# Kernel optimization log

Measured on AMD Instinct MI355X. Metric: run time of the kernel, lower is better.

The kernel has to match this reference:

```python
import jax, jax.numpy as jnp
import numpy as np

B = 2048   # batch
C = 64     # EEG channels (num_eegch)
T = 125    # time samples -> pool5 -> 25 -> (p=5, 5)
H = 8      # num_heads
L = 6      # num_layers
D = 16     # num_projected_features
QK = 8     # qkv_len
P = 5      # tokens before cls
EPS = 1e-5


def setup_inputs() -> dict:
    key = jax.random.key(0)
    ks = iter(jax.random.split(key, 64))

    def nrm(shape, s=0.05):
        return jax.random.normal(next(ks), shape, jnp.float32) * s

    return {
        "x": jax.random.normal(next(ks), (B, 1, C, T), jnp.float32),
        "conv_t_w": nrm((8, 1, 1, 63)),
        "conv_t_b": nrm((8,)),
        "bn1_g": 1.0 + nrm((8,)),
        "bn1_b": nrm((8,)),
        "bn1_m": nrm((8,)),
        "bn1_v": 1.0 + 0.1 * jax.random.uniform(next(ks), (8,), jnp.float32),
        "conv_s_w": nrm((16, 1, C, 1)),
        "conv_s_b": nrm((16,)),
        "bn2_g": 1.0 + nrm((16,)),
        "bn2_b": nrm((16,)),
        "bn2_m": nrm((16,)),
        "bn2_v": 1.0 + 0.1 * jax.random.uniform(next(ks), (16,), jnp.float32),
        "proj_w": nrm((D, 16 * 5)),
        "proj_b": nrm((D,)),
        "cls_token": nrm((1, 1, D), 1.0),
        "pe": nrm((1, P + 1, D), 1.0),
        "qkv_w": nrm((L, 3 * H * QK, D)),
        "qkv_b": nrm((L, 3 * H * QK)),
        "out_w": nrm((L, D, H * QK)),
        "out_b": nrm((L, D)),
        "ln1_g": jnp.ones((L, D), jnp.float32),
        "ln1_b": jnp.zeros((L, D), jnp.float32),
        "ln2_g": jnp.ones((L, D), jnp.float32),
        "ln2_b": jnp.zeros((L, D), jnp.float32),
        "mlp_w1": nrm((L, 2 * D, D)),
        "mlp_b1": nrm((L, 2 * D)),
        "mlp_w2": nrm((L, D, 2 * D)),
        "mlp_b2": nrm((L, D)),
        "head_ln_g": jnp.ones((D,), jnp.float32),
        "head_ln_b": jnp.zeros((D,), jnp.float32),
        "head_w": nrm((2, D)),
        "head_b": nrm((2,)),
    }


def _bn(z, g, b, m, v):
    s = (g * jax.lax.rsqrt(v + EPS))[None, :, None, None]
    return (z - m[None, :, None, None]) * s + b[None, :, None, None]


def _ln(z, g, b):
    m = z.mean(-1, keepdims=True)
    var = jnp.mean((z - m) ** 2, -1, keepdims=True)
    return (z - m) * jax.lax.rsqrt(var + EPS) * g + b


def _forward(x, conv_t_w, conv_t_b, bn1_g, bn1_b, bn1_m, bn1_v,
             conv_s_w, conv_s_b, bn2_g, bn2_b, bn2_m, bn2_v,
             proj_w, proj_b, cls_token, pe,
             qkv_w, qkv_b, out_w, out_b, ln1_g, ln1_b, ln2_g, ln2_b,
             mlp_w1, mlp_b1, mlp_w2, mlp_b2,
             head_ln_g, head_ln_b, head_w, head_b):
    b = x.shape[0]
    dn = ('NCHW', 'OIHW', 'NCHW')
    # temporal conv, 'same' padding on width (kernel 63 -> pad 31/31)
    y = jax.lax.conv_general_dilated(x, conv_t_w, (1, 1), [(0, 0), (31, 31)], dimension_numbers=dn)
    y = _bn(y + conv_t_b[None, :, None, None], bn1_g, bn1_b, bn1_m, bn1_v)
    # grouped spatial conv collapses the EEG-channel axis
    y = jax.lax.conv_general_dilated(y, conv_s_w, (1, 1), 'VALID', dimension_numbers=dn, feature_group_count=8)
    y = _bn(y + conv_s_b[None, :, None, None], bn2_g, bn2_b, bn2_m, bn2_v)
    y = jax.nn.elu(y)                              # (b,16,1,125)
    y = y.reshape(b, 16, 1, T // 5, 5).mean(-1)    # avg_pool2d (1,5) -> (b,16,1,25)
    # dropout: identity at inference
    y = y.reshape(b, 16, 1, P, 5)
    y = jnp.swapaxes(y, 3, 4)
    tok = jnp.swapaxes(y.reshape(b, 16 * 5, P), 1, 2)   # (b,5,80)
    tok = tok @ proj_w.T + proj_b                       # (b,5,16)
    z = jnp.concatenate([jnp.broadcast_to(cls_token, (b, 1, D)), tok], axis=1) + pe  # (b,6,16)
    scale = QK ** -0.5
    for i in range(L):
        h1 = _ln(z, ln1_g[i], ln1_b[i])
        qkv = h1 @ qkv_w[i].T + qkv_b[i]                # (b,6,3*H*QK)
        q, k, v = jnp.split(qkv, 3, axis=-1)
        q = q.reshape(b, P + 1, H, QK).transpose(0, 2, 1, 3)
        k = k.reshape(b, P + 1, H, QK).transpose(0, 2, 1, 3)
        v = v.reshape(b, P + 1, H, QK).transpose(0, 2, 1, 3)
        att = jax.nn.softmax(jnp.einsum('bhsd,bhtd->bhst', q, k) * scale, axis=-1)
        o = jnp.einsum('bhst,bhtd->bhsd', att, v).transpose(0, 2, 1, 3).reshape(b, P + 1, H * QK)
        z = o @ out_w[i].T + out_b[i] + z
        h2 = _ln(z, ln2_g[i], ln2_b[i])
        m = jax.nn.gelu(h2 @ mlp_w1[i].T + mlp_b1[i], approximate=False) @ mlp_w2[i].T + mlp_b2[i]
        z = m + z
    cls = _ln(z[:, 0, :], head_ln_g, head_ln_b)
    return jax.nn.softmax(cls @ head_w.T + head_b, axis=-1)


def reference(x, conv_t_w, conv_t_b, bn1_g, bn1_b, bn1_m, bn1_v,
              conv_s_w, conv_s_b, bn2_g, bn2_b, bn2_m, bn2_v,
              proj_w, proj_b, cls_token, pe,
              qkv_w, qkv_b, out_w, out_b, ln1_g, ln1_b, ln2_g, ln2_b,
              mlp_w1, mlp_b1, mlp_w2, mlp_b2,
              head_ln_g, head_ln_b, head_w, head_b):
    return _forward(x, conv_t_w, conv_t_b, bn1_g, bn1_b, bn1_m, bn1_v,
                    conv_s_w, conv_s_b, bn2_g, bn2_b, bn2_m, bn2_v,
                    proj_w, proj_b, cls_token, pe,
                    qkv_w, qkv_b, out_w, out_b, ln1_g, ln1_b, ln2_g, ln2_b,
                    mlp_w1, mlp_b1, mlp_w2, mlp_b2,
                    head_ln_g, head_ln_b, head_w, head_b)
```

## Files before the change

### kernel.cpp

```cpp
#include <hip/hip_runtime.h>

#define WAVE_SYNC() do { asm volatile("" ::: "memory"); \
                         __builtin_amdgcn_wave_barrier(); \
                         asm volatile("" ::: "memory"); } while (0)

typedef _Float16 h2 __attribute__((ext_vector_type(2)));
typedef _Float16 h4 __attribute__((ext_vector_type(4)));
typedef _Float16 h8 __attribute__((ext_vector_type(8)));

__device__ __forceinline__ float fdot2(h2 a, h2 b, float c) {
#if defined(__has_builtin)
#if __has_builtin(__builtin_amdgcn_fdot2)
    return __builtin_amdgcn_fdot2(a, b, c, false);
#else
    return (float)a[0]*(float)b[0] + (float)a[1]*(float)b[1] + c;
#endif
#else
    return (float)a[0]*(float)b[0] + (float)a[1]*(float)b[1] + c;
#endif
}

__device__ __forceinline__ float dot8h(h8 a, h8 b, float c) {
    float s = c;
    #pragma unroll
    for (int i = 0; i < 4; ++i) {
        h2 x = {a[2*i], a[2*i+1]};
        h2 y = {b[2*i], b[2*i+1]};
        s = fdot2(x, y, s);
    }
    return s;
}

__device__ __forceinline__ float dot16h(h8 a0, h8 a1, h8 b0, h8 b1, float c) {
    return dot8h(a1, b1, dot8h(a0, b0, c));
}

__device__ __forceinline__ float ln_norm16(float z, float g, float bb) {
    float s = z, q = z * z;
    #pragma unroll
    for (int off = 8; off >= 1; off >>= 1) {
        s += __shfl_xor(s, off, 16);
        q += __shfl_xor(q, off, 16);
    }
    float mean = s * 0.0625f;
    float var  = q * 0.0625f - mean * mean;
    return (z - mean) * rsqrtf(var + 1e-5f) * g + bb;
}

__device__ __forceinline__ float gelu_exact(float a) {
    float xa = fabsf(a) * 0.70710678118654752f;
    float tt = 1.f / (1.f + 0.3275911f * xa);
    float poly = tt * (0.254829592f + tt * (-0.284496736f + tt * (1.421413741f
               + tt * (-1.453152027f + tt * 1.061405429f))));
    float erfv = 1.f - poly * __expf(-xa * xa);
    erfv = a >= 0.f ? erfv : -erfv;
    return 0.5f * a * (1.f + erfv);
}

#define FS_XSTR 210
#define FS_PF   1680
#define FS_TOTF 2128

extern "C" __global__ __launch_bounds__(128, 2)
void eegnet_frontend(
    const float* __restrict__ x,
    const float* __restrict__ conv_t_w, const float* __restrict__ conv_t_b,
    const float* __restrict__ bn1_g, const float* __restrict__ bn1_b,
    const float* __restrict__ bn1_m, const float* __restrict__ bn1_v,
    const float* __restrict__ conv_s_w, const float* __restrict__ conv_s_b,
    const float* __restrict__ bn2_g, const float* __restrict__ bn2_b,
    const float* __restrict__ bn2_m, const float* __restrict__ bn2_v,
    const float* __restrict__ proj_w, const float* __restrict__ proj_b,
    float* __restrict__ tokws)
{
    __shared__ __align__(16) float sm[FS_TOTF];
    _Float16* smh = reinterpret_cast<_Float16*>(sm);
    const int b   = blockIdx.x;
    const int tid = threadIdx.x;

    for (int i = tid; i < 16 * 85; i += 128) {
        int row = i / 85, k = i - row * 85;
        int off = (k < 32) ? k : (k + 125);
        smh[row * FS_XSTR + off] = (_Float16)0.f;
    }

    if (tid < 125) {
        const float* xb = x + (size_t)b * 8000 + tid;
        float acc[16];
        #pragma unroll
        for (int o = 0; o < 16; ++o) acc[o] = 0.f;
        #pragma unroll 8
        for (int c = 0; c < 64; ++c) {
            float xv = xb[c * 125];
            #pragma unroll
            for (int o = 0; o < 16; ++o)
                acc[o] += conv_s_w[o * 64 + c] * xv;
        }
        #pragma unroll
        for (int o = 0; o < 16; ++o)
            smh[o * FS_XSTR + 32 + tid] = (_Float16)acc[o];
    }

    __syncthreads();

    const int oo = tid & 15, qg = tid >> 4, gg = oo >> 1;
    float sa, cc;
    {
        float s1 = bn1_g[gg] * rsqrtf(bn1_v[gg] + 1e-5f);
        float b1 = (conv_t_b[gg] - bn1_m[gg]) * s1 + bn1_b[gg];
        float s2 = bn2_g[oo] * rsqrtf(bn2_v[oo] + 1e-5f);
        float ssum = 0.f;
        const float4* csw = reinterpret_cast<const float4*>(conv_s_w + oo * 64);
        #pragma unroll
        for (int i = 0; i < 16; ++i) {
            float4 v = csw[i];
            ssum += v.x + v.y + v.z + v.w;
        }
        sa = s1 * s2;
        cc = (b1 * ssum + conv_s_b[oo] - bn2_m[oo]) * s2 + bn2_b[oo];
    }
    float wt[63];
    #pragma unroll
    for (int k = 0; k < 63; ++k) wt[k] = conv_t_w[gg * 63 + k];

    #pragma unroll 2
    for (int jj = 0; jj < 4; ++jj) {
        int j  = qg * 4 + jj;
        int jc = min(j, 24);
        int base = oo * FS_XSTR + 5 * jc + 1;
        float acc5[5] = {0.f, 0.f, 0.f, 0.f, 0.f};
        #pragma unroll
        for (int m = 0; m < 67; ++m) {
            float xv = (float)smh[base + m];
            #pragma unroll
            for (int u = 0; u < 5; ++u)
                if (u <= m && m - u <= 62) acc5[u] += wt[m - u] * xv;
        }
        float psum = 0.f;
        #pragma unroll
        for (int u = 0; u < 5; ++u) {
            float v = acc5[u] * sa + cc;
            psum += (v > 0.f) ? v : (__expf(v) - 1.f);
        }
        if (j == jc) sm[FS_PF + oo * 28 + j] = psum * 0.2f;
    }

    __syncthreads();

    if (tid < 80) {
        int p = tid >> 4, dd = tid & 15;
        float acc = proj_b[dd];
        const float4* wp = reinterpret_cast<const float4*>(proj_w + dd * 80);
        #pragma unroll
        for (int i = 0; i < 20; ++i) {
            float4 w4 = wp[i];
            acc += w4.x * sm[FS_PF + ((4*i+0)/5) * 28 + p * 5 + ((4*i+0)%5)];
            acc += w4.y * sm[FS_PF + ((4*i+1)/5) * 28 + p * 5 + ((4*i+1)%5)];
            acc += w4.z * sm[FS_PF + ((4*i+2)/5) * 28 + p * 5 + ((4*i+2)%5)];
            acc += w4.w * sm[FS_PF + ((4*i+3)/5) * 28 + p * 5 + ((4*i+3)%5)];
        }
        tokws[b * 80 + p * 16 + dd] = acc;
    }
}

#define WQKVH 0
#define WOUTH 4608
#define WM1H  5760
#define WM2H  6528
#define BQKVF 3584
#define BOUTF 3776
#define BM1F  3792
#define BM2F  3824
#define LN1GF 3840
#define LN1BF 3856
#define LN2GF 3872
#define LN2BF 3888
#define SCR0  7808
#define SSTRH 1584
#define SH1H  0
#define SQKVH 144
#define SMHSH 1344
#define T_BYTES 28288

extern "C" __global__ __launch_bounds__(256, 2)
void eegnet_transformer(
    const float* __restrict__ cls_token, const float* __restrict__ pe,
    const float* __restrict__ qkv_w, const float* __restrict__ qkv_b,
    const float* __restrict__ out_w, const float* __restrict__ out_b,
    const float* __restrict__ ln1_g, const float* __restrict__ ln1_b,
    const float* __restrict__ ln2_g, const float* __restrict__ ln2_b,
    const float* __restrict__ mlp_w1, const float* __restrict__ mlp_b1,
    const float* __restrict__ mlp_w2, const float* __restrict__ mlp_b2,
    const float* __restrict__ head_ln_g, const float* __restrict__ head_ln_b,
    const float* __restrict__ head_w, const float* __restrict__ head_b,
    const float* __restrict__ tokws, float* __restrict__ out)
{
    __shared__ __align__(16) unsigned char smb[T_BYTES];
    float*    smf = reinterpret_cast<float*>(smb);
    _Float16* smh = reinterpret_cast<_Float16*>(smb);

    const int tid = threadIdx.x;
    const int ss  = tid >> 7;
    const int u   = tid & 127;
    const int sA  = blockIdx.x * 4 + ss * 2;
    const int d16 = u & 15, qg = u >> 4;
    const int t6c = min(qg, 5);
    const int wav = u >> 6, al = u & 63;
    const int sbA = SCR0 + (ss * 2    ) * SSTRH;
    const int sbB = SCR0 + (ss * 2 + 1) * SSTRH;

    float zA, zB;
    {
        float peV = pe[t6c * 16 + d16];
        if (t6c == 0) {
            float cv = cls_token[d16];
            zA = cv + peV; zB = cv + peV;
        } else {
            zA = tokws[(sA    ) * 80 + (t6c - 1) * 16 + d16] + peV;
            zB = tokws[(sA + 1) * 80 + (t6c - 1) * 16 + d16] + peV;
        }
    }

    #pragma unroll 1
    for (int li = 0; li < 6; ++li) {
        __syncthreads();

        {
            const float4* s1 = reinterpret_cast<const float4*>(qkv_w + li * 3072);
            #pragma unroll
            for (int it = 0; it < 3; ++it) {
                int i = tid + it * 256;
                float4 v = s1[i];
                int j = i >> 2, k = (i & 3) << 2;
                h4 hv = {(_Float16)v.x, (_Float16)v.y, (_Float16)v.z, (_Float16)v.w};
                *reinterpret_cast<h4*>(&smh[WQKVH + j * 24 + k]) = hv;
            }
            {
                float4 v = reinterpret_cast<const float4*>(out_w + li * 1024)[tid];
                int j = tid >> 4, k = (tid & 15) << 2;
                h4 hv = {(_Float16)v.x, (_Float16)v.y, (_Float16)v.z, (_Float16)v.w};
                *reinterpret_cast<h4*>(&smh[WOUTH + j * 72 + k]) = hv;
            }
            if (tid < 128) {
                float4 v = reinterpret_cast<const float4*>(mlp_w1 + li * 512)[tid];
                int j = tid >> 2, k = (tid & 3) << 2;
                h4 hv = {(_Float16)v.x, (_Float16)v.y, (_Float16)v.z, (_Float16)v.w};
                *reinterpret_cast<h4*>(&smh[WM1H + j * 24 + k]) = hv;
            } else {
                int i = tid - 128;
                float4 v = reinterpret_cast<const float4*>(mlp_w2 + li * 512)[i];
                int j = i >> 3, k = (i & 7) << 2;
                h4 hv = {(_Float16)v.x, (_Float16)v.y, (_Float16)v.z, (_Float16)v.w};
                *reinterpret_cast<h4*>(&smh[WM2H + j * 40 + k]) = hv;
            }
            if (tid < 192) smf[BQKVF + tid] = qkv_b[li * 192 + tid];
            else if (tid < 208) smf[BOUTF + tid - 192] = out_b[li * 16 + tid - 192];
            else if (tid < 240) smf[BM1F + tid - 208]  = mlp_b1[li * 32 + tid - 208];
            else               smf[BM2F + tid - 240]  = mlp_b2[li * 16 + tid - 240];
            if (tid >= 64 && tid < 80)        smf[LN1GF + tid - 64]  = ln1_g[li * 16 + tid - 64];
            else if (tid >= 80 && tid < 96)   smf[LN1BF + tid - 80]  = ln1_b[li * 16 + tid - 80];
            else if (tid >= 96 && tid < 112)  smf[LN2GF + tid - 96]  = ln2_g[li * 16 + tid - 96];
            else if (tid >= 112 && tid < 128) smf[LN2BF + tid - 112] = ln2_b[li * 16 + tid - 112];
        }
        __syncthreads();

        {
            float g = smf[LN1GF + d16], bb = smf[LN1BF + d16];
            smh[sbA + SH1H + t6c * 24 + d16] = (_Float16)ln_norm16(zA, g, bb);
            smh[sbB + SH1H + t6c * 24 + d16] = (_Float16)ln_norm16(zB, g, bb);
        }
        WAVE_SYNC();

        h8 hA0 = *reinterpret_cast<const h8*>(&smh[sbA + SH1H + t6c * 24]);
        h8 hA1 = *reinterpret_cast<const h8*>(&smh[sbA + SH1H + t6c * 24 + 8]);
        h8 hB0 = *reinterpret_cast<const h8*>(&smh[sbB + SH1H + t6c * 24]);
        h8 hB1 = *reinterpret_cast<const h8*>(&smh[sbB + SH1H + t6c * 24 + 8]);

        #pragma unroll 2
        for (int r = 0; r < 12; ++r) {
            int j = d16 + 16 * r;
            h8 w0 = *reinterpret_cast<const h8*>(&smh[WQKVH + j * 24]);
            h8 w1 = *reinterpret_cast<const h8*>(&smh[WQKVH + j * 24 + 8]);
            float bb = smf[BQKVF + j];
            smh[sbA + SQKVH + t6c * 200 + j] = (_Float16)dot16h(hA0, hA1, w0, w1, bb);
            smh[sbB + SQKVH + t6c * 200 + j] = (_Float16)dot16h(hB0, hB1, w0, w1, bb);
        }
        __syncthreads();

        {
            bool act = (wav == 0) ? (al < 32) : (al < 16);
            if (act) {
                int h  = al & 7;
                int qs = (wav == 0) ? (al >> 3) : 4 + (al >> 3);
                const int qoffA = sbA + SQKVH + qs * 200 + h * 8;
                const int qoffB = sbB + SQKVH + qs * 200 + h * 8;
                h8 qA = *reinterpret_cast<const h8*>(&smh[qoffA]);
                h8 qB = *reinterpret_cast<const h8*>(&smh[qoffB]);
                float scA[6], scB[6];
                #pragma unroll
                for (int t = 0; t < 6; ++t) {
                    h8 kA = *reinterpret_cast<const h8*>(&smh[sbA + SQKVH + t * 200 + 64 + h * 8]);
                    h8 kB = *reinterpret_cast<const h8*>(&smh[sbB + SQKVH + t * 200 + 64 + h * 8]);
                    scA[t] = dot8h(qA, kA, 0.f) * 0.35355339059327373f;
                    scB[t] = dot8h(qB, kB, 0.f) * 0.35355339059327373f;
                }
                float mxA = scA[0], mxB = scB[0];
                #pragma unroll
                for (int t = 1; t < 6; ++t) { mxA = fmaxf(mxA, scA[t]); mxB = fmaxf(mxB, scB[t]); }
                float suA = 0.f, suB = 0.f;
                #pragma unroll
                for (int t = 0; t < 6; ++t) {
                    scA[t] = __expf(scA[t] - mxA); suA += scA[t];
                    scB[t] = __expf(scB[t] - mxB); suB += scB[t];
                }
                float ivA = 1.f / suA, ivB = 1.f / suB;
                h2 oA[4], oB[4];
                #pragma unroll
                for (int k2 = 0; k2 < 4; ++k2) { oA[k2] = h2{0, 0}; oB[k2] = h2{0, 0}; }
                #pragma unroll
                for (int t = 0; t < 6; ++t) {
                    h8 vA = *reinterpret_cast<const h8*>(&smh[sbA + SQKVH + t * 200 + 128 + h * 8]);
                    h8 vB = *reinterpret_cast<const h8*>(&smh[sbB + SQKVH + t * 200 + 128 + h * 8]);
                    _Float16 aa = (_Float16)(scA[t] * ivA);
                    _Float16 ab = (_Float16)(scB[t] * ivB);
                    h2 av = {aa, aa}, bv = {ab, ab};
                    #pragma unroll
                    for (int k2 = 0; k2 < 4; ++k2) {
                        h2 va = {vA[2*k2], vA[2*k2+1]};
                        h2 vb = {vB[2*k2], vB[2*k2+1]};
                        oA[k2] += av * va;
                        oB[k2] += bv * vb;
                    }
                }
                h8 stA, stB;
                #pragma unroll
                for (int k2 = 0; k2 < 4; ++k2) {
                    stA[2*k2] = oA[k2][0]; stA[2*k2+1] = oA[k2][1];
                    stB[2*k2] = oB[k2][0]; stB[2*k2+1] = oB[k2][1];
                }
                *reinterpret_cast<h8*>(&smh[qoffA]) = stA;
                *reinterpret_cast<h8*>(&smh[qoffB]) = stB;
            }
        }
        WAVE_SYNC();

        {
            float aA = smf[BOUTF + d16], aB = aA;
            #pragma unroll
            for (int i = 0; i < 8; ++i) {
                h8 w  = *reinterpret_cast<const h8*>(&smh[WOUTH + d16 * 72 + 8 * i]);
                h8 va = *reinterpret_cast<const h8*>(&smh[sbA + SQKVH + t6c * 200 + 8 * i]);
                h8 vb = *reinterpret_cast<const h8*>(&smh[sbB + SQKVH + t6c * 200 + 8 * i]);
                aA = dot8h(va, w, aA);
                aB = dot8h(vb, w, aB);
            }
            zA += aA; zB += aB;
        }

        {
            float g = smf[LN2GF + d16], bb = smf[LN2BF + d16];
            smh[sbA + SH1H + t6c * 24 + d16] = (_Float16)ln_norm16(zA, g, bb);
            smh[sbB + SH1H + t6c * 24 + d16] = (_Float16)ln_norm16(zB, g, bb);
        }
        WAVE_SYNC();
        hA0 = *reinterpret_cast<const h8*>(&smh[sbA + SH1H + t6c * 24]);
        hA1 = *reinterpret_cast<const h8*>(&smh[sbA + SH1H + t6c * 24 + 8]);
        hB0 = *reinterpret_cast<const h8*>(&smh[sbB + SH1H + t6c * 24]);
        hB1 = *reinterpret_cast<const h8*>(&smh[sbB + SH1H + t6c * 24 + 8]);

        #pragma unroll
        for (int r = 0; r < 2; ++r) {
            int uu = d16 + 16 * r;
            h8 w0 = *reinterpret_cast<const h8*>(&smh[WM1H + uu * 24]);
            h8 w1 = *reinterpret_cast<const h8*>(&smh[WM1H + uu * 24 + 8]);
            float bb = smf[BM1F + uu];
            float aA = dot16h(hA0, hA1, w0, w1, bb);
            float aB = dot16h(hB0, hB1, w0, w1, bb);
            smh[sbA + SMHSH + t6c * 40 + uu] = (_Float16)gelu_exact(aA);
            smh[sbB + SMHSH + t6c * 40 + uu] = (_Float16)gelu_exact(aB);
        }
        WAVE_SYNC();

        {
            float aA = smf[BM2F + d16], aB = aA;
            #pragma unroll
            for (int i = 0; i < 4; ++i) {
                h8 w  = *reinterpret_cast<const h8*>(&smh[WM2H + d16 * 40 + 8 * i]);
                h8 va = *reinterpret_cast<const h8*>(&smh[sbA + SMHSH + t6c * 40 + 8 * i]);
                h8 vb = *reinterpret_cast<const h8*>(&smh[sbB + SMHSH + t6c * 40 + 8 * i]);
                aA = dot8h(va, w, aA);
                aB = dot8h(vb, w, aB);
            }
            zA += aA; zB += aB;
        }
    }

    if (u < 16) {
        float g = head_ln_g[d16], bb = head_ln_b[d16];
        float w0 = head_w[d16], w1 = head_w[16 + d16];
        float cvA = ln_norm16(zA, g, bb);
        float cvB = ln_norm16(zB, g, bb);
        float pA0 = cvA * w0, pA1 = cvA * w1;
        float pB0 = cvB * w0, pB1 = cvB * w1;
        #pragma unroll
        for (int off = 8; off >= 1; off >>= 1) {
            pA0 += __shfl_xor(pA0, off, 16);
            pA1 += __shfl_xor(pA1, off, 16);
            pB0 += __shfl_xor(pB0, off, 16);
            pB1 += __shfl_xor(pB1, off, 16);
        }
        if (u == 0) {
            float hb0 = head_b[0], hb1 = head_b[1];
            {
                float l0 = pA0 + hb0, l1 = pA1 + hb1;
                float mx = fmaxf(l0, l1);
                float e0 = __expf(l0 - mx), e1 = __expf(l1 - mx);
                float inv = 1.f / (e0 + e1);
                out[sA * 2 + 0] = e0 * inv;
                out[sA * 2 + 1] = e1 * inv;
            }
            {
                float l0 = pB0 + hb0, l1 = pB1 + hb1;
                float mx = fmaxf(l0, l1);
                float e0 = __expf(l0 - mx), e1 = __expf(l1 - mx);
                float inv = 1.f / (e0 + e1);
                out[(sA + 1) * 2 + 0] = e0 * inv;
                out[(sA + 1) * 2 + 1] = e1 * inv;
            }
        }
    }
}

extern "C" void kernel_launch(void* const* d_in, const int* in_sizes, int n_in,
                              void* d_out, int out_size, void* d_ws, size_t ws_size,
                              hipStream_t stream) {
    (void)n_in; (void)ws_size; (void)out_size;
    const float* a0  = (const float*)d_in[0];
    const float* a1  = (const float*)d_in[1];
    const float* a2  = (const float*)d_in[2];
    const float* a3  = (const float*)d_in[3];
    const float* a4  = (const float*)d_in[4];
    const float* a5  = (const float*)d_in[5];
    const float* a6  = (const float*)d_in[6];
    const float* a7  = (const float*)d_in[7];
    const float* a8  = (const float*)d_in[8];
    const float* a9  = (const float*)d_in[9];
    const float* a10 = (const float*)d_in[10];
    const float* a11 = (const float*)d_in[11];
    const float* a12 = (const float*)d_in[12];
    const float* a13 = (const float*)d_in[13];
    const float* a14 = (const float*)d_in[14];
    const float* a15 = (const float*)d_in[15];
    const float* a16 = (const float*)d_in[16];
    const float* a17 = (const float*)d_in[17];
    const float* a18 = (const float*)d_in[18];
    const float* a19 = (const float*)d_in[19];
    const float* a20 = (const float*)d_in[20];
    const float* a21 = (const float*)d_in[21];
    const float* a22 = (const float*)d_in[22];
    const float* a23 = (const float*)d_in[23];
    const float* a24 = (const float*)d_in[24];
    const float* a25 = (const float*)d_in[25];
    const float* a26 = (const float*)d_in[26];
    const float* a27 = (const float*)d_in[27];
    const float* a28 = (const float*)d_in[28];
    const float* a29 = (const float*)d_in[29];
    const float* a30 = (const float*)d_in[30];
    const float* a31 = (const float*)d_in[31];
    const float* a32 = (const float*)d_in[32];

    int Bn = in_sizes[0] / (64 * 125);
    float* tokws = (float*)d_ws;

    eegnet_frontend<<<Bn, 128, 0, stream>>>(
        a0, a1, a2, a3, a4, a5, a6, a7, a8, a9, a10, a11, a12, a13, a14, tokws);

    eegnet_transformer<<<Bn / 4, 256, 0, stream>>>(
        a15, a16, a17, a18, a19, a20, a21, a22, a23, a24, a25, a26, a27, a28,
        a29, a30, a31, a32, tokws, (float*)d_out);
}
```

Before: 243.8 us.

## Stage input in LDS as fp16 for spatial conv; one sample per transformer block

The frontend now loads the whole per-sample input with vectorized float4 reads into shared memory as fp16. It also stages the spatial conv weights there and computes the channel conv with fdot2 instead of strided scalar global loads. The transformer kernel is restructured from 4 samples per 256-thread block (2 per thread) down to 1 sample per 128-thread block, with 4x more blocks. This trades weight-loading amortization across samples for more blocks and less LDS per block, and it lowers precision of the spatial conv inputs to fp16.

Result: no change. 240.0 us (-1.6%).

```diff
diff --git a/kernel.cpp b/kernel.cpp
--- a/kernel.cpp
+++ b/kernel.cpp
@@ -57,9 +57,10 @@
     return 0.5f * a * (1.f + erfv);
 }
 
-#define FS_XSTR 210
-#define FS_PF   1680
-#define FS_TOTF 2128
+#define F5_XSTR 210
+#define F5_PF   1680
+#define F5_WLH  8000
+#define F5_TOTF 4512
 
 extern "C" __global__ __launch_bounds__(128, 2)
 void eegnet_frontend(
@@ -73,34 +74,67 @@
     const float* __restrict__ proj_w, const float* __restrict__ proj_b,
     float* __restrict__ tokws)
 {
-    __shared__ __align__(16) float sm[FS_TOTF];
+    __shared__ __align__(16) float sm[F5_TOTF];
     _Float16* smh = reinterpret_cast<_Float16*>(sm);
     const int b   = blockIdx.x;
     const int tid = threadIdx.x;
 
+    {
+        const float4* xb4 = reinterpret_cast<const float4*>(x + (size_t)b * 8000);
+        #pragma unroll
+        for (int k = 0; k < 16; ++k) {
+            int g = min(tid + k * 128, 1999);
+            float4 v = xb4[g];
+            h4 hv = {(_Float16)v.x, (_Float16)v.y, (_Float16)v.z, (_Float16)v.w};
+            *reinterpret_cast<h4*>(&smh[4 * g]) = hv;
+        }
+    }
+    {
+        #pragma unroll
+        for (int k = 0; k < 4; ++k) {
+            int i  = tid + k * 128;
+            int c2 = i & 31, o = i >> 5;
+            float2 wv = *reinterpret_cast<const float2*>(conv_s_w + o * 64 + 2 * c2);
+            h2 hp = {(_Float16)wv.x, (_Float16)wv.y};
+            *reinterpret_cast<h2*>(&smh[F5_WLH + (c2 * 16 + o) * 2]) = hp;
+        }
+    }
+    __syncthreads();
+
+    float acc[16];
+    #pragma unroll
+    for (int o = 0; o < 16; ++o) acc[o] = 0.f;
+    if (tid < 125) {
+        #pragma unroll 4
+        for (int c2 = 0; c2 < 32; ++c2) {
+            h2 xp = { smh[(2 * c2) * 125 + tid], smh[(2 * c2 + 1) * 125 + tid] };
+            const h8* wrow = reinterpret_cast<const h8*>(&smh[F5_WLH + c2 * 32]);
+            h8 w0 = wrow[0], w1 = wrow[1], w2 = wrow[2], w3 = wrow[3];
+            #pragma unroll
+            for (int o = 0; o < 4; ++o) {
+                h2 p0 = {w0[2*o], w0[2*o+1]};
+                h2 p1 = {w1[2*o], w1[2*o+1]};
+                h2 p2 = {w2[2*o], w2[2*o+1]};
+                h2 p3 = {w3[2*o], w3[2*o+1]};
+                acc[o]      = fdot2(p0, xp, acc[o]);
+                acc[4 + o]  = fdot2(p1, xp, acc[4 + o]);
+                acc[8 + o]  = fdot2(p2, xp, acc[8 + o]);
+                acc[12 + o] = fdot2(p3, xp, acc[12 + o]);
+            }
+        }
+    }
+    __syncthreads();
+
     for (int i = tid; i < 16 * 85; i += 128) {
         int row = i / 85, k = i - row * 85;
         int off = (k < 32) ? k : (k + 125);
-        smh[row * FS_XSTR + off] = (_Float16)0.f;
-    }
-
+        smh[row * F5_XSTR + off] = (_Float16)0.f;
+    }
     if (tid < 125) {
-        const float* xb = x + (size_t)b * 8000 + tid;
-        float acc[16];
-        #pragma unroll
-        for (int o = 0; o < 16; ++o) acc[o] = 0.f;
-        #pragma unroll 8
-        for (int c = 0; c < 64; ++c) {
-            float xv = xb[c * 125];
-            #pragma unroll
-            for (int o = 0; o < 16; ++o)
-                acc[o] += conv_s_w[o * 64 + c] * xv;
-        }
         #pragma unroll
         for (int o = 0; o < 16; ++o)
-            smh[o * FS_XSTR + 32 + tid] = (_Float16)acc[o];
-    }
-
+            smh[o * F5_XSTR + 32 + tid] = (_Float16)acc[o];
+    }
     __syncthreads();
 
     const int oo = tid & 15, qg = tid >> 4, gg = oo >> 1;
@@ -127,7 +161,7 @@
     for (int jj = 0; jj < 4; ++jj) {
         int j  = qg * 4 + jj;
         int jc = min(j, 24);
-        int base = oo * FS_XSTR + 5 * jc + 1;
+        int base = oo * F5_XSTR + 5 * jc + 1;
         float acc5[5] = {0.f, 0.f, 0.f, 0.f, 0.f};
         #pragma unroll
         for (int m = 0; m < 67; ++m) {
@@ -142,24 +176,24 @@
             float v = acc5[u] * sa + cc;
             psum += (v > 0.f) ? v : (__expf(v) - 1.f);
         }
-        if (j == jc) sm[FS_PF + oo * 28 + j] = psum * 0.2f;
+        if (j == jc) sm[F5_PF + oo * 28 + j] = psum * 0.2f;
     }
 
     __syncthreads();
 
     if (tid < 80) {
         int p = tid >> 4, dd = tid & 15;
-        float acc = proj_b[dd];
+        float acc3 = proj_b[dd];
         const float4* wp = reinterpret_cast<const float4*>(proj_w + dd * 80);
         #pragma unroll
         for (int i = 0; i < 20; ++i) {
             float4 w4 = wp[i];
-            acc += w4.x * sm[FS_PF + ((4*i+0)/5) * 28 + p * 5 + ((4*i+0)%5)];
-            acc += w4.y * sm[FS_PF + ((4*i+1)/5) * 28 + p * 5 + ((4*i+1)%5)];
-            acc += w4.z * sm[FS_PF + ((4*i+2)/5) * 28 + p * 5 + ((4*i+2)%5)];
-            acc += w4.w * sm[FS_PF + ((4*i+3)/5) * 28 + p * 5 + ((4*i+3)%5)];
-        }
-        tokws[b * 80 + p * 16 + dd] = acc;
+            acc3 += w4.x * sm[F5_PF + ((4*i+0)/5) * 28 + p * 5 + ((4*i+0)%5)];
+            acc3 += w4.y * sm[F5_PF + ((4*i+1)/5) * 28 + p * 5 + ((4*i+1)%5)];
+            acc3 += w4.z * sm[F5_PF + ((4*i+2)/5) * 28 + p * 5 + ((4*i+2)%5)];
+            acc3 += w4.w * sm[F5_PF + ((4*i+3)/5) * 28 + p * 5 + ((4*i+3)%5)];
+        }
+        tokws[b * 80 + p * 16 + dd] = acc3;
     }
 }
 
@@ -180,9 +214,9 @@
 #define SH1H  0
 #define SQKVH 144
 #define SMHSH 1344
-#define T_BYTES 28288
-
-extern "C" __global__ __launch_bounds__(256, 2)
+#define T_BYTES 18784
+
+extern "C" __global__ __launch_bounds__(128, 2)
 void eegnet_transformer(
     const float* __restrict__ cls_token, const float* __restrict__ pe,
     const float* __restrict__ qkv_w, const float* __restrict__ qkv_b,
@@ -200,25 +234,17 @@
     _Float16* smh = reinterpret_cast<_Float16*>(smb);
 
     const int tid = threadIdx.x;
-    const int ss  = tid >> 7;
-    const int u   = tid & 127;
-    const int sA  = blockIdx.x * 4 + ss * 2;
-    const int d16 = u & 15, qg = u >> 4;
+    const int sA  = blockIdx.x;
+    const int d16 = tid & 15, qg = tid >> 4;
     const int t6c = min(qg, 5);
-    const int wav = u >> 6, al = u & 63;
-    const int sbA = SCR0 + (ss * 2    ) * SSTRH;
-    const int sbB = SCR0 + (ss * 2 + 1) * SSTRH;
-
-    float zA, zB;
+    const int wav = tid >> 6, al = tid & 63;
+    const int sb  = SCR0;
+
+    float zA;
     {
         float peV = pe[t6c * 16 + d16];
-        if (t6c == 0) {
-            float cv = cls_token[d16];
-            zA = cv + peV; zB = cv + peV;
-        } else {
-            zA = tokws[(sA    ) * 80 + (t6c - 1) * 16 + d16] + peV;
-            zB = tokws[(sA + 1) * 80 + (t6c - 1) * 16 + d16] + peV;
-        }
+        if (t6c == 0) zA = cls_token[d16] + peV;
+        else          zA = tokws[sA * 80 + (t6c - 1) * 16 + d16] + peV;
     }
 
     #pragma unroll 1
@@ -228,35 +254,42 @@
         {
             const float4* s1 = reinterpret_cast<const float4*>(qkv_w + li * 3072);
             #pragma unroll
-            for (int it = 0; it < 3; ++it) {
-                int i = tid + it * 256;
+            for (int it = 0; it < 6; ++it) {
+                int i = tid + it * 128;
                 float4 v = s1[i];
                 int j = i >> 2, k = (i & 3) << 2;
                 h4 hv = {(_Float16)v.x, (_Float16)v.y, (_Float16)v.z, (_Float16)v.w};
                 *reinterpret_cast<h4*>(&smh[WQKVH + j * 24 + k]) = hv;
             }
-            {
-                float4 v = reinterpret_cast<const float4*>(out_w + li * 1024)[tid];
-                int j = tid >> 4, k = (tid & 15) << 2;
+            const float4* s2 = reinterpret_cast<const float4*>(out_w + li * 1024);
+            #pragma unroll
+            for (int it = 0; it < 2; ++it) {
+                int i = tid + it * 128;
+                float4 v = s2[i];
+                int j = i >> 4, k = (i & 15) << 2;
                 h4 hv = {(_Float16)v.x, (_Float16)v.y, (_Float16)v.z, (_Float16)v.w};
                 *reinterpret_cast<h4*>(&smh[WOUTH + j * 72 + k]) = hv;
             }
-            if (tid < 128) {
+            {
                 float4 v = reinterpret_cast<const float4*>(mlp_w1 + li * 512)[tid];
                 int j = tid >> 2, k = (tid & 3) << 2;
                 h4 hv = {(_Float16)v.x, (_Float16)v.y, (_Float16)v.z, (_Float16)v.w};
                 *reinterpret_cast<h4*>(&smh[WM1H + j * 24 + k]) = hv;
-            } else {
-                int i = tid - 128;
-                float4 v = reinterpret_cast<const float4*>(mlp_w2 + li * 512)[i];
-                int j = i >> 3, k = (i & 7) << 2;
+            }
+            {
+                float4 v = reinterpret_cast<const float4*>(mlp_w2 + li * 512)[tid];
+                int j = tid >> 3, k = (tid & 7) << 2;
                 h4 hv = {(_Float16)v.x, (_Float16)v.y, (_Float16)v.z, (_Float16)v.w};
                 *reinterpret_cast<h4*>(&smh[WM2H + j * 40 + k]) = hv;
             }
-            if (tid < 192) smf[BQKVF + tid] = qkv_b[li * 192 + tid];
-            else if (tid < 208) smf[BOUTF + tid - 192] = out_b[li * 16 + tid - 192];
-            else if (tid < 240) smf[BM1F + tid - 208]  = mlp_b1[li * 32 + tid - 208];
-            else               smf[BM2F + tid - 240]  = mlp_b2[li * 16 + tid - 240];
+            #pragma unroll
+            for (int p = 0; p < 2; ++p) {
+                int i = tid + p * 128;
+                if (i < 192)       smf[BQKVF + i]       = qkv_b[li * 192 + i];
+                else if (i < 208)  smf[BOUTF + i - 192] = out_b[li * 16 + i - 192];
+                else if (i < 240)  smf[BM1F + i - 208]  = mlp_b1[li * 32 + i - 208];
+                else               smf[BM2F + i - 240]  = mlp_b2[li * 16 + i - 240];
+            }
             if (tid >= 64 && tid < 80)        smf[LN1GF + tid - 64]  = ln1_g[li * 16 + tid - 64];
             else if (tid >= 80 && tid < 96)   smf[LN1BF + tid - 80]  = ln1_b[li * 16 + tid - 80];
             else if (tid >= 96 && tid < 112)  smf[LN2GF + tid - 96]  = ln2_g[li * 16 + tid - 96];
@@ -266,15 +299,12 @@
 
         {
             float g = smf[LN1GF + d16], bb = smf[LN1BF + d16];
-            smh[sbA + SH1H + t6c * 24 + d16] = (_Float16)ln_norm16(zA, g, bb);
-            smh[sbB + SH1H + t6c * 24 + d16] = (_Float16)ln_norm16(zB, g, bb);
+            smh[sb + SH1H + t6c * 24 + d16] = (_Float16)ln_norm16(zA, g, bb);
         }
         WAVE_SYNC();
 
-        h8 hA0 = *reinterpret_cast<const h8*>(&smh[sbA + SH1H + t6c * 24]);
-        h8 hA1 = *reinterpret_cast<const h8*>(&smh[sbA + SH1H + t6c * 24 + 8]);
-        h8 hB0 = *reinterpret_cast<const h8*>(&smh[sbB + SH1H + t6c * 24]);
-        h8 hB1 = *reinterpret_cast<const h8*>(&smh[sbB + SH1H + t6c * 24 + 8]);
+        h8 hA0 = *reinterpret_cast<const h8*>(&smh[sb + SH1H + t6c * 24]);
+        h8 hA1 = *reinterpret_cast<const h8*>(&smh[sb + SH1H + t6c * 24 + 8]);
 
         #pragma unroll 2
         for (int r = 0; r < 12; ++r) {
@@ -282,8 +312,7 @@
             h8 w0 = *reinterpret_cast<const h8*>(&smh[WQKVH + j * 24]);
             h8 w1 = *reinterpret_cast<const h8*>(&smh[WQKVH + j * 24 + 8]);
             float bb = smf[BQKVF + j];
-            smh[sbA + SQKVH + t6c * 200 + j] = (_Float16)dot16h(hA0, hA1, w0, w1, bb);
-            smh[sbB + SQKVH + t6c * 200 + j] = (_Float16)dot16h(hB0, hB1, w0, w1, bb);
+            smh[sb + SQKVH + t6c * 200 + j] = (_Float16)dot16h(hA0, hA1, w0, w1, bb);
         }
         __syncthreads();
 
@@ -292,81 +321,63 @@
             if (act) {
                 int h  = al & 7;
                 int qs = (wav == 0) ? (al >> 3) : 4 + (al >> 3);
-                const int qoffA = sbA + SQKVH + qs * 200 + h * 8;
-                const int qoffB = sbB + SQKVH + qs * 200 + h * 8;
-                h8 qA = *reinterpret_cast<const h8*>(&smh[qoffA]);
-                h8 qB = *reinterpret_cast<const h8*>(&smh[qoffB]);
-                float scA[6], scB[6];
+                const int qoff = sb + SQKVH + qs * 200 + h * 8;
+                h8 qA = *reinterpret_cast<const h8*>(&smh[qoff]);
+                float scA[6];
                 #pragma unroll
                 for (int t = 0; t < 6; ++t) {
-                    h8 kA = *reinterpret_cast<const h8*>(&smh[sbA + SQKVH + t * 200 + 64 + h * 8]);
-                    h8 kB = *reinterpret_cast<const h8*>(&smh[sbB + SQKVH + t * 200 + 64 + h * 8]);
+                    h8 kA = *reinterpret_cast<const h8*>(&smh[sb + SQKVH + t * 200 + 64 + h * 8]);
                     scA[t] = dot8h(qA, kA, 0.f) * 0.35355339059327373f;
-                    scB[t] = dot8h(qB, kB, 0.f) * 0.35355339059327373f;
                 }
-                float mxA = scA[0], mxB = scB[0];
-                #pragma unroll
-                for (int t = 1; t < 6; ++t) { mxA = fmaxf(mxA, scA[t]); mxB = fmaxf(mxB, scB[t]); }
-                float suA = 0.f, suB = 0.f;
+                float mxA = scA[0];
+                #pragma unroll
+                for (int t = 1; t < 6; ++t) mxA = fmaxf(mxA, scA[t]);
+                float suA = 0.f;
+                #pragma unroll
+                for (int t = 0; t < 6; ++t) { scA[t] = __expf(scA[t] - mxA); suA += scA[t]; }
+                float ivA = 1.f / suA;
+                h2 oA[4];
+                #pragma unroll
+                for (int k2 = 0; k2 < 4; ++k2) oA[k2] = h2{0, 0};
                 #pragma unroll
                 for (int t = 0; t < 6; ++t) {
-                    scA[t] = __expf(scA[t] - mxA); suA += scA[t];
-                    scB[t] = __expf(scB[t] - mxB); suB += scB[t];
-                }
-                float ivA = 1.f / suA, ivB = 1.f / suB;
-                h2 oA[4], oB[4];
-                #pragma unroll
-                for (int k2 = 0; k2 < 4; ++k2) { oA[k2] = h2{0, 0}; oB[k2] = h2{0, 0}; }
-                #pragma unroll
-                for (int t = 0; t < 6; ++t) {
-                    h8 vA = *reinterpret_cast<const h8*>(&smh[sbA + SQKVH + t * 200 + 128 + h * 8]);
-                    h8 vB = *reinterpret_cast<const h8*>(&smh[sbB + SQKVH + t * 200 + 128 + h * 8]);
+                    h8 vA = *reinterpret_cast<const h8*>(&smh[sb + SQKVH + t * 200 + 128 + h * 8]);
                     _Float16 aa = (_Float16)(scA[t] * ivA);
-                    _Float16 ab = (_Float16)(scB[t] * ivB);
-                    h2 av = {aa, aa}, bv = {ab, ab};
+                    h2 av = {aa, aa};
                     #pragma unroll
                     for (int k2 = 0; k2 < 4; ++k2) {
                         h2 va = {vA[2*k2], vA[2*k2+1]};
-                        h2 vb = {vB[2*k2], vB[2*k2+1]};
                         oA[k2] += av * va;
-                        oB[k2] += bv * vb;
                     }
                 }
-                h8 stA, stB;
+                h8 stA;
                 #pragma unroll
                 for (int k2 = 0; k2 < 4; ++k2) {
                     stA[2*k2] = oA[k2][0]; stA[2*k2+1] = oA[k2][1];
-                    stB[2*k2] = oB[k2][0]; stB[2*k2+1] = oB[k2][1];
                 }
-                *reinterpret_cast<h8*>(&smh[qoffA]) = stA;
-                *reinterpret_cast<h8*>(&smh[qoffB]) = stB;
+                *reinterpret_cast<h8*>(&smh[qoff]) = stA;
             }
         }
         WAVE_SYNC();
 
         {
-            float aA = smf[BOUTF + d16], aB = aA;
+            float aA = smf[BOUTF + d16];
             #pragma unroll
             for (int i = 0; i < 8; ++i) {
                 h8 w  = *reinterpret_cast<const h8*>(&smh[WOUTH + d16 * 72 + 8 * i]);
-                h8 va = *reinterpret_cast<const h8*>(&smh[sbA + SQKVH + t6c * 200 + 8 * i]);
-                h8 vb = *reinterpret_cast<const h8*>(&smh[sbB + SQKVH + t6c * 200 + 8 * i]);
+                h8 va = *reinterpret_cast<const h8*>(&smh[sb + SQKVH + t6c * 200 + 8 * i]);
                 aA = dot8h(va, w, aA);
-                aB = dot8h(vb, w, aB);
-            }
-            zA += aA; zB += aB;
+            }
+            zA += aA;
         }
 
         {
             float g = smf[LN2GF + d16], bb = smf[LN2BF + d16];
-            smh[sbA + SH1H + t6c * 24 + d16] = (_Float16)ln_norm16(zA, g, bb);
-            smh[sbB + SH1H + t6c * 24 + d16] = (_Float16)ln_norm16(zB, g, bb);
+            smh[sb + SH1H + t6c * 24 + d16] = (_Float16)ln_norm16(zA, g, bb);
         }
         WAVE_SYNC();
-        hA0 = *reinterpret_cast<const h8*>(&smh[sbA + SH1H + t6c * 24]);
-        hA1 = *reinterpret_cast<const h8*>(&smh[sbA + SH1H + t6c * 24 + 8]);
-        hB0 = *reinterpret_cast<const h8*>(&smh[sbB + SH1H + t6c * 24]);
-        hB1 = *reinterpret_cast<const h8*>(&smh[sbB + SH1H + t6c * 24 + 8]);
+        hA0 = *reinterpret_cast<const h8*>(&smh[sb + SH1H + t6c * 24]);
+        hA1 = *reinterpret_cast<const h8*>(&smh[sb + SH1H + t6c * 24 + 8]);
 
         #pragma unroll
         for (int r = 0; r < 2; ++r) {
@@ -375,58 +386,39 @@
             h8 w1 = *reinterpret_cast<const h8*>(&smh[WM1H + uu * 24 + 8]);
             float bb = smf[BM1F + uu];
             float aA = dot16h(hA0, hA1, w0, w1, bb);
-            float aB = dot16h(hB0, hB1, w0, w1, bb);
-            smh[sbA + SMHSH + t6c * 40 + uu] = (_Float16)gelu_exact(aA);
-            smh[sbB + SMHSH + t6c * 40 + uu] = (_Float16)gelu_exact(aB);
+            smh[sb + SMHSH + t6c * 40 + uu] = (_Float16)gelu_exact(aA);
         }
         WAVE_SYNC();
 
         {
-            float aA = smf[BM2F + d16], aB = aA;
+            float aA = smf[BM2F + d16];
             #pragma unroll
             for (int i = 0; i < 4; ++i) {
                 h8 w  = *reinterpret_cast<const h8*>(&smh[WM2H + d16 * 40 + 8 * i]);
-                h8 va = *reinterpret_cast<const h8*>(&smh[sbA + SMHSH + t6c * 40 + 8 * i]);
-                h8 vb = *reinterpret_cast<const h8*>(&smh[sbB + SMHSH + t6c * 40 + 8 * i]);
+                h8 va = *reinterpret_cast<const h8*>(&smh[sb + SMHSH + t6c * 40 + 8 * i]);
                 aA = dot8h(va, w, aA);
-                aB = dot8h(vb, w, aB);
-            }
-            zA += aA; zB += aB;
-        }
-    }
-
-    if (u < 16) {
+            }
+            zA += aA;
+        }
+    }
+
+    if (tid < 16) {
         float g = head_ln_g[d16], bb = head_ln_b[d16];
         float w0 = head_w[d16], w1 = head_w[16 + d16];
         float cvA = ln_norm16(zA, g, bb);
-        float cvB = ln_norm16(zB, g, bb);
         float pA0 = cvA * w0, pA1 = cvA * w1;
-        float pB0 = cvB * w0, pB1 = cvB * w1;
         #pragma unroll
         for (int off = 8; off >= 1; off >>= 1) {
             pA0 += __shfl_xor(pA0, off, 16);
             pA1 += __shfl_xor(pA1, off, 16);
-            pB0 += __shfl_xor(pB0, off, 16);
-            pB1 += __shfl_xor(pB1, off, 16);
-        }
-        if (u == 0) {
-            float hb0 = head_b[0], hb1 = head_b[1];
-            {
-                float l0 = pA0 + hb0, l1 = pA1 + hb1;
-                float mx = fmaxf(l0, l1);
-                float e0 = __expf(l0 - mx), e1 = __expf(l1 - mx);
-                float inv = 1.f / (e0 + e1);
-                out[sA * 2 + 0] = e0 * inv;
-                out[sA * 2 + 1] = e1 * inv;
-            }
-            {
-                float l0 = pB0 + hb0, l1 = pB1 + hb1;
-                float mx = fmaxf(l0, l1);
-                float e0 = __expf(l0 - mx), e1 = __expf(l1 - mx);
-                float inv = 1.f / (e0 + e1);
-                out[(sA + 1) * 2 + 0] = e0 * inv;
-                out[(sA + 1) * 2 + 1] = e1 * inv;
-            }
+        }
+        if (tid == 0) {
+            float l0 = pA0 + head_b[0], l1 = pA1 + head_b[1];
+            float mx = fmaxf(l0, l1);
+            float e0 = __expf(l0 - mx), e1 = __expf(l1 - mx);
+            float inv = 1.f / (e0 + e1);
+            out[sA * 2 + 0] = e0 * inv;
+            out[sA * 2 + 1] = e1 * inv;
         }
     }
 }
@@ -475,7 +467,7 @@
     eegnet_frontend<<<Bn, 128, 0, stream>>>(
         a0, a1, a2, a3, a4, a5, a6, a7, a8, a9, a10, a11, a12, a13, a14, tokws);
 
-    eegnet_transformer<<<Bn / 4, 256, 0, stream>>>(
+    eegnet_transformer<<<Bn, 128, 0, stream>>>(
         a15, a16, a17, a18, a19, a20, a21, a22, a23, a24, a25, a26, a27, a28,
         a29, a30, a31, a32, tokws, (float*)d_out);
 }
```
